# Kernel optimization log

Hardware: AMD Instinct MI355X
Metric: run time of the kernel (lower is better)

Reference implementation:

```python
import jax, jax.numpy as jnp
import numpy as np

BN_EPS = 1e-5


def setup_inputs() -> dict:
    key = jax.random.key(0)
    ks = jax.random.split(key, 3)
    B, S, C, H, W = 4, 8, 64, 96, 96
    P = 6
    DIM = 768
    x = jax.random.normal(ks[0], (B, S, C, H, W), dtype=jnp.float32)
    conv_w = jax.random.normal(ks[1], (C, C, 3, 3), dtype=jnp.float32) * 0.05
    conv_b = jnp.zeros((C,), dtype=jnp.float32)
    bn_gamma = jnp.ones((C,), dtype=jnp.float32)
    bn_beta = jnp.zeros((C,), dtype=jnp.float32)
    bn_mean = jnp.zeros((C,), dtype=jnp.float32)
    bn_var = jnp.ones((C,), dtype=jnp.float32)
    proj_w = jax.random.normal(ks[2], (DIM, P * P * C), dtype=jnp.float32) * 0.02
    proj_b = jnp.zeros((DIM,), dtype=jnp.float32)
    mask = jnp.ones((P, P), dtype=jnp.float32)
    return {"x": x, "conv_w": conv_w, "conv_b": conv_b,
            "bn_gamma": bn_gamma, "bn_beta": bn_beta,
            "bn_mean": bn_mean, "bn_var": bn_var,
            "proj_w": proj_w, "proj_b": proj_b,
            "mask": mask, "patch_size": P}


def reference(x, conv_w, conv_b, bn_gamma, bn_beta, bn_mean, bn_var,
              proj_w, proj_b, mask, patch_size):
    B, S, C, H, W = x.shape
    p = patch_size
    Cout = conv_w.shape[0]
    # Fuse the per-frame loop: run conv over all B*S frames at once.
    xf = x.reshape(B * S, C, H, W)
    y = jax.lax.conv_general_dilated(
        xf, conv_w, window_strides=(1, 1), padding=[(1, 1), (1, 1)],
        dimension_numbers=("NCHW", "OIHW", "NCHW"))
    y = y + conv_b[None, :, None, None]
    # BatchNorm2d (eval-mode running stats); Dropout2d is identity at eval.
    inv = jax.lax.rsqrt(bn_var + BN_EPS)
    y = (y - bn_mean[None, :, None, None]) * (bn_gamma * inv)[None, :, None, None] \
        + bn_beta[None, :, None, None]
    y = jax.nn.gelu(y, approximate=False)  # torch GELU default = exact erf
    y = y.reshape(B, S, Cout, H, W)
    # Patch extraction, row-major over (l_idx, r_idx) exactly as the loop.
    pr = H // p  # patches per row
    patches = y.reshape(B, S, Cout, pr, p, pr, p).transpose(0, 1, 3, 5, 2, 4, 6)
    patches = patches.reshape(B, S, pr * pr, Cout, p, p) * mask  # [B,S,P,C,p,p]
    # Flatten(start_dim=2 on [B,S,C,p,p]) + Linear + GELU, batched over patches.
    flat = patches.reshape(B, S, pr * pr, Cout * p * p)
    tokens = jax.nn.gelu(
        jnp.einsum("bsnf,df->bsnd", flat, proj_w) + proj_b, approximate=False)
    return tokens, patches
```

## Files before the change

kernel.cpp:

```cpp
#include <hip/hip_runtime.h>
#include <hip/hip_bf16.h>
#include <math.h>


typedef unsigned short u16;
typedef __bf16 bf16x8 __attribute__((ext_vector_type(8)));
typedef float f32x4 __attribute__((ext_vector_type(4)));

#define NFRM 32
#define CH 64
#define HW 96
#define HWP 98
#define KP 2304
#define DIMN 768
#define MTOK 8192
#define TOKN (MTOK * DIMN)
#define NPAT (MTOK * KP)
#define XHWC_ELEMS ((size_t)NFRM * HWP * HWP * CH)
#define BP_OFF XHWC_ELEMS
#define PW_OFF (BP_OFF + 36864)

static __device__ __forceinline__ u16 f2b(float f) {
  unsigned u = __builtin_bit_cast(unsigned, f);
  u += 0x7fffu + ((u >> 16) & 1u);
  return (u16)(u >> 16);
}
static __device__ __forceinline__ float gelu_f(float x) {
  return 0.5f * x * (1.0f + erff(x * 0.7071067811865476f));
}

__global__ __launch_bounds__(256) void k_transpose(const float* __restrict__ x,
                                                   u16* __restrict__ xhwc) {
  __shared__ u16 tile[96 * 66];
  const int f = blockIdx.x / 96, h = blockIdx.x % 96;
  const int t = threadIdx.x;
  const float* xp = x + (size_t)f * CH * HW * HW + (size_t)h * HW;
#pragma unroll
  for (int k = 0; k < 6; ++k) {
    int e = (k * 256 + t) * 4;
    int ci = e / 96, w = e % 96;
    float4 v = *(const float4*)(xp + (size_t)ci * (HW * HW) + w);
    tile[(w + 0) * 66 + ci] = f2b(v.x);
    tile[(w + 1) * 66 + ci] = f2b(v.y);
    tile[(w + 2) * 66 + ci] = f2b(v.z);
    tile[(w + 3) * 66 + ci] = f2b(v.w);
  }
  __syncthreads();
  u16* op = xhwc + ((size_t)(f * HWP + h + 1) * HWP + 1) * CH;
#pragma unroll
  for (int k = 0; k < 12; ++k) {
    int e2 = (k * 256 + t) * 2;
    int w = e2 >> 6, ci = e2 & 63;
    *(unsigned*)(op + e2) = *(const unsigned*)(&tile[w * 66 + ci]);
  }
}

__global__ __launch_bounds__(256) void k_bpack(const float* __restrict__ w,
                                               u16* __restrict__ bp) {
  int e = blockIdx.x * 256 + threadIdx.x;
  int co = e / 576, r = e - co * 576, tap = r >> 6, ci = r & 63;
  bp[e] = f2b(w[(co * 64 + ci) * 9 + tap]);
}

__global__ __launch_bounds__(256) void k_pw(const float* __restrict__ pw,
                                            u16* __restrict__ dst) {
  int e = (blockIdx.x * 256 + threadIdx.x) * 4;
  float4 v = *(const float4*)(pw + e);
  ushort4 o;
  o.x = f2b(v.x); o.y = f2b(v.y); o.z = f2b(v.z); o.w = f2b(v.w);
  *(ushort4*)(dst + e) = o;
}

__global__ __launch_bounds__(256) void k_conv(
    const u16* __restrict__ xhwc, const u16* __restrict__ bw,
    const float* __restrict__ cb, const float* __restrict__ gma,
    const float* __restrict__ bta, const float* __restrict__ mu,
    const float* __restrict__ var, const float* __restrict__ msk,
    float* __restrict__ pout) {
  __shared__ u16 As[128 * 72];
  __shared__ u16 Bs[64 * 72];
  const int f = blockIdx.x / 72;
  const int m0 = (blockIdx.x % 72) * 128;
  const int t = threadIdx.x;
  const int wv = t >> 6, l = t & 63, quad = l >> 4, lm = l & 15;

  const int r = t >> 1, c0 = (t & 1) * 32;
  const int mg = m0 + r;
  const int np = mg / 36, ii = mg - np * 36;
  const int hb = (np >> 4) * 6 + ii / 6;
  const int wb = (np & 15) * 6 + (ii % 6);
  const u16* xf = xhwc + (size_t)f * (HWP * HWP * CH);
  const int bco = t >> 2, bc = (t & 3) * 16;

  f32x4 acc[2][4];
#pragma unroll
  for (int s = 0; s < 2; ++s)
#pragma unroll
    for (int u = 0; u < 4; ++u) acc[s][u] = (f32x4){0.f, 0.f, 0.f, 0.f};

  for (int tap = 0; tap < 9; ++tap) {
    const int di = tap / 3, dj = tap - di * 3;
    __syncthreads();
    const u16* src = xf + ((hb + di) * HWP + (wb + dj)) * CH + c0;
    u16* dA = &As[r * 72 + c0];
    *(uint4*)(dA + 0) = *(const uint4*)(src + 0);
    *(uint4*)(dA + 8) = *(const uint4*)(src + 8);
    *(uint4*)(dA + 16) = *(const uint4*)(src + 16);
    *(uint4*)(dA + 24) = *(const uint4*)(src + 24);
    const u16* bsrc = bw + bco * 576 + tap * 64 + bc;
    u16* dB = &Bs[bco * 72 + bc];
    *(uint4*)(dB + 0) = *(const uint4*)(bsrc + 0);
    *(uint4*)(dB + 8) = *(const uint4*)(bsrc + 8);
    __syncthreads();
#pragma unroll
    for (int ks = 0; ks < 2; ++ks) {
      const int ko = ks * 32 + quad * 8;
      bf16x8 a0 = *(const bf16x8*)&As[(wv * 32 + lm) * 72 + ko];
      bf16x8 a1 = *(const bf16x8*)&As[(wv * 32 + 16 + lm) * 72 + ko];
#pragma unroll
      for (int u = 0; u < 4; ++u) {
        bf16x8 b = *(const bf16x8*)&Bs[(u * 16 + lm) * 72 + ko];
        acc[0][u] = __builtin_amdgcn_mfma_f32_16x16x32_bf16(a0, b, acc[0][u], 0, 0, 0);
        acc[1][u] = __builtin_amdgcn_mfma_f32_16x16x32_bf16(a1, b, acc[1][u], 0, 0, 0);
      }
    }
  }
  const int mwb = m0 + wv * 32;
#pragma unroll
  for (int u = 0; u < 4; ++u) {
    const int co = u * 16 + lm;
    const float scv = gma[co] * rsqrtf(var[co] + 1e-5f);
    const float b2v = (cb[co] - mu[co]) * scv + bta[co];
#pragma unroll
    for (int s = 0; s < 2; ++s) {
#pragma unroll
      for (int rg = 0; rg < 4; ++rg) {
        const int ml = mwb + s * 16 + quad * 4 + rg;
        const int n = ml / 36, jj = ml - n * 36;
        float v = acc[s][u][rg] * scv + b2v;
        v = gelu_f(v) * msk[jj];
        pout[((size_t)(f * 256 + n) * 64 + co) * 36 + jj] = v;
      }
    }
  }
}

__global__ __launch_bounds__(256) void k_cvt(const float* __restrict__ pat,
                                             u16* __restrict__ abf) {
  int e = (blockIdx.x * 256 + threadIdx.x) * 4;
  float4 v = *(const float4*)(pat + e);
  ushort4 o;
  o.x = f2b(v.x); o.y = f2b(v.y); o.z = f2b(v.z); o.w = f2b(v.w);
  *(ushort4*)(abf + e) = o;
}

__global__ __launch_bounds__(256) void k_gemm(const u16* __restrict__ A,
                                              const u16* __restrict__ Bt,
                                              const float* __restrict__ pb,
                                              float* __restrict__ out) {
  __shared__ u16 As[128 * 40];
  __shared__ u16 Bs[64 * 40];
  const int bn = blockIdx.x % 12, bm = blockIdx.x / 12;
  const int m0 = bm * 128, n0 = bn * 64;
  const int t = threadIdx.x, wv = t >> 6, l = t & 63, quad = l >> 4, lm = l & 15;
  const int ar = t >> 2, ac = (t & 3) * 8;

  f32x4 acc[2][4];
#pragma unroll
  for (int s = 0; s < 2; ++s)
#pragma unroll
    for (int u = 0; u < 4; ++u) acc[s][u] = (f32x4){0.f, 0.f, 0.f, 0.f};

  for (int k0 = 0; k0 < KP; k0 += 32) {
    __syncthreads();
    *(uint4*)&As[ar * 40 + ac] = *(const uint4*)&A[(size_t)(m0 + ar) * KP + k0 + ac];
    *(uint4*)&As[(ar + 64) * 40 + ac] =
        *(const uint4*)&A[(size_t)(m0 + ar + 64) * KP + k0 + ac];
    *(uint4*)&Bs[ar * 40 + ac] = *(const uint4*)&Bt[(size_t)(n0 + ar) * KP + k0 + ac];
    __syncthreads();
    const int ko = quad * 8;
    bf16x8 a0 = *(const bf16x8*)&As[(wv * 32 + lm) * 40 + ko];
    bf16x8 a1 = *(const bf16x8*)&As[(wv * 32 + 16 + lm) * 40 + ko];
#pragma unroll
    for (int u = 0; u < 4; ++u) {
      bf16x8 b = *(const bf16x8*)&Bs[(u * 16 + lm) * 40 + ko];
      acc[0][u] = __builtin_amdgcn_mfma_f32_16x16x32_bf16(a0, b, acc[0][u], 0, 0, 0);
      acc[1][u] = __builtin_amdgcn_mfma_f32_16x16x32_bf16(a1, b, acc[1][u], 0, 0, 0);
    }
  }
#pragma unroll
  for (int u = 0; u < 4; ++u) {
    const int n = n0 + u * 16 + lm;
    const float bias = pb[n];
#pragma unroll
    for (int s = 0; s < 2; ++s) {
#pragma unroll
      for (int rg = 0; rg < 4; ++rg) {
        const int m = m0 + wv * 32 + s * 16 + quad * 4 + rg;
        out[(size_t)m * DIMN + n] = gelu_f(acc[s][u][rg] + bias);
      }
    }
  }
}

extern "C" void kernel_launch(void* const* d_in, const int* in_sizes, int n_in,
                              void* d_out, int out_size, void* d_ws, size_t ws_size,
                              hipStream_t stream) {
  const float* x = (const float*)d_in[0];
  const float* conv_w = (const float*)d_in[1];
  const float* conv_b = (const float*)d_in[2];
  const float* bn_gamma = (const float*)d_in[3];
  const float* bn_beta = (const float*)d_in[4];
  const float* bn_mean = (const float*)d_in[5];
  const float* bn_var = (const float*)d_in[6];
  const float* proj_w = (const float*)d_in[7];
  const float* proj_b = (const float*)d_in[8];
  const float* mask = (const float*)d_in[9];
  float* out = (float*)d_out;
  float* patches = out + TOKN;
  u16* ws = (u16*)d_ws;
  u16* xhwc = ws;
  u16* bp = ws + BP_OFF;
  u16* pw = ws + PW_OFF;

  hipMemsetAsync(d_ws, 0, XHWC_ELEMS * sizeof(u16), stream);
  k_transpose<<<NFRM * HW, 256, 0, stream>>>(x, xhwc);
  k_bpack<<<144, 256, 0, stream>>>(conv_w, bp);
  k_pw<<<1728, 256, 0, stream>>>(proj_w, pw);
  k_conv<<<NFRM * 72, 256, 0, stream>>>(xhwc, bp, conv_b, bn_gamma, bn_beta,
                                        bn_mean, bn_var, mask, patches);
  k_cvt<<<18432, 256, 0, stream>>>(patches, xhwc);
  k_gemm<<<64 * 12, 256, 0, stream>>>(xhwc, pw, proj_b, out);
}
```

Before: 329.9 us.

## Restructure conv to stage full halo row-band in LDS and use direct global-to-LDS loads

The conv kernel now loads an 8-row by 98-column halo band of the padded NHWC input once into XOR-swizzled LDS using global_load_lds. It then reuses that band across all 9 taps with 512-thread blocks and a larger per-wave tile, so input pixels are no longer re-fetched from global memory for every tap. Conv weights are staged in two tap blocks. The projection GEMM also switches its A/B tile staging to direct global-to-LDS loads with unpadded LDS rows. The larger LDS footprint and register tile may limit occupancy, and the unpadded GEMM tiles may cause LDS bank conflicts.

```diff
diff --git a/kernel.cpp b/kernel.cpp
--- a/kernel.cpp
+++ b/kernel.cpp
@@ -19,6 +19,7 @@
 #define XHWC_ELEMS ((size_t)NFRM * HWP * HWP * CH)
 #define BP_OFF XHWC_ELEMS
 #define PW_OFF (BP_OFF + 36864)
+#define BSTR 328
 
 static __device__ __forceinline__ u16 f2b(float f) {
   unsigned u = __builtin_bit_cast(unsigned, f);
@@ -27,6 +28,12 @@
 }
 static __device__ __forceinline__ float gelu_f(float x) {
   return 0.5f * x * (1.0f + erff(x * 0.7071067811865476f));
+}
+
+typedef __attribute__((address_space(3))) unsigned int lds_uint;
+typedef __attribute__((address_space(1))) const unsigned int g_uint;
+static __device__ __forceinline__ void gload16(const u16* g, u16* s) {
+  __builtin_amdgcn_global_load_lds((g_uint*)g, (lds_uint*)s, 16, 0, 0);
 }
 
 __global__ __launch_bounds__(256) void k_transpose(const float* __restrict__ x,
@@ -71,73 +78,88 @@
   *(ushort4*)(dst + e) = o;
 }
 
-__global__ __launch_bounds__(256) void k_conv(
+template <int T0, int NT>
+static __device__ __forceinline__ void conv_tapblock(
+    const u16* __restrict__ bw, u16* Bs2, const char* asb,
+    f32x4 (&acc)[9][2], const int (&pb)[9],
+    const int t, const int wn, const int lm, const int quad) {
+  for (int e = t; e < 64 * NT * 8; e += 512) {
+    const int co = e / (NT * 8), kk = e - co * (NT * 8);
+    *(uint4*)&Bs2[co * BSTR + kk * 8] = *(const uint4*)&bw[co * 576 + T0 * 64 + kk * 8];
+  }
+  __syncthreads();
+#pragma unroll
+  for (int tp = 0; tp < NT; ++tp) {
+    const int tap = T0 + tp;
+    const int di = tap / 3, dj = tap - (tap / 3) * 3;
+#pragma unroll
+    for (int ks = 0; ks < 2; ++ks) {
+      const int kq = ks * 4 + quad;
+      const bf16x8 b0 = *(const bf16x8*)&Bs2[(wn * 32 + lm) * BSTR + tp * 64 + ks * 32 + quad * 8];
+      const bf16x8 b1 = *(const bf16x8*)&Bs2[(wn * 32 + 16 + lm) * BSTR + tp * 64 + ks * 32 + quad * 8];
+#pragma unroll
+      for (int mf = 0; mf < 9; ++mf) {
+        const int p = pb[mf] + di * 98 + dj;
+        const bf16x8 a = *(const bf16x8*)(asb + p * 128 + ((kq ^ (p & 7)) << 4));
+        acc[mf][0] = __builtin_amdgcn_mfma_f32_16x16x32_bf16(a, b0, acc[mf][0], 0, 0, 0);
+        acc[mf][1] = __builtin_amdgcn_mfma_f32_16x16x32_bf16(a, b1, acc[mf][1], 0, 0, 0);
+      }
+    }
+  }
+}
+
+__global__ __launch_bounds__(512, 2) void k_conv(
     const u16* __restrict__ xhwc, const u16* __restrict__ bw,
     const float* __restrict__ cb, const float* __restrict__ gma,
     const float* __restrict__ bta, const float* __restrict__ mu,
     const float* __restrict__ var, const float* __restrict__ msk,
     float* __restrict__ pout) {
-  __shared__ u16 As[128 * 72];
-  __shared__ u16 Bs[64 * 72];
-  const int f = blockIdx.x / 72;
-  const int m0 = (blockIdx.x % 72) * 128;
+  __shared__ alignas(16) u16 As2[8 * 98 * 64];
+  __shared__ alignas(16) u16 Bs2[64 * BSTR];
+  const int f = blockIdx.x >> 4, pr0 = blockIdx.x & 15;
   const int t = threadIdx.x;
-  const int wv = t >> 6, l = t & 63, quad = l >> 4, lm = l & 15;
-
-  const int r = t >> 1, c0 = (t & 1) * 32;
-  const int mg = m0 + r;
-  const int np = mg / 36, ii = mg - np * 36;
-  const int hb = (np >> 4) * 6 + ii / 6;
-  const int wb = (np & 15) * 6 + (ii % 6);
-  const u16* xf = xhwc + (size_t)f * (HWP * HWP * CH);
-  const int bco = t >> 2, bc = (t & 3) * 16;
-
-  f32x4 acc[2][4];
-#pragma unroll
-  for (int s = 0; s < 2; ++s)
-#pragma unroll
-    for (int u = 0; u < 4; ++u) acc[s][u] = (f32x4){0.f, 0.f, 0.f, 0.f};
-
-  for (int tap = 0; tap < 9; ++tap) {
-    const int di = tap / 3, dj = tap - di * 3;
-    __syncthreads();
-    const u16* src = xf + ((hb + di) * HWP + (wb + dj)) * CH + c0;
-    u16* dA = &As[r * 72 + c0];
-    *(uint4*)(dA + 0) = *(const uint4*)(src + 0);
-    *(uint4*)(dA + 8) = *(const uint4*)(src + 8);
-    *(uint4*)(dA + 16) = *(const uint4*)(src + 16);
-    *(uint4*)(dA + 24) = *(const uint4*)(src + 24);
-    const u16* bsrc = bw + bco * 576 + tap * 64 + bc;
-    u16* dB = &Bs[bco * 72 + bc];
-    *(uint4*)(dB + 0) = *(const uint4*)(bsrc + 0);
-    *(uint4*)(dB + 8) = *(const uint4*)(bsrc + 8);
-    __syncthreads();
-#pragma unroll
-    for (int ks = 0; ks < 2; ++ks) {
-      const int ko = ks * 32 + quad * 8;
-      bf16x8 a0 = *(const bf16x8*)&As[(wv * 32 + lm) * 72 + ko];
-      bf16x8 a1 = *(const bf16x8*)&As[(wv * 32 + 16 + lm) * 72 + ko];
-#pragma unroll
-      for (int u = 0; u < 4; ++u) {
-        bf16x8 b = *(const bf16x8*)&Bs[(u * 16 + lm) * 72 + ko];
-        acc[0][u] = __builtin_amdgcn_mfma_f32_16x16x32_bf16(a0, b, acc[0][u], 0, 0, 0);
-        acc[1][u] = __builtin_amdgcn_mfma_f32_16x16x32_bf16(a1, b, acc[1][u], 0, 0, 0);
-      }
-    }
-  }
-  const int mwb = m0 + wv * 32;
-#pragma unroll
-  for (int u = 0; u < 4; ++u) {
-    const int co = u * 16 + lm;
+  const int wid = t >> 6, l = t & 63, quad = l >> 4, lm = l & 15;
+  const int wm = wid >> 1, wn = wid & 1;
+
+  const u16* sbase = xhwc + ((size_t)f * HWP + pr0 * 6) * (HWP * CH);
+  for (int c = wid; c < 98; c += 8) {
+    const int p = c * 8 + (l >> 3);
+    const int g = (l & 7) ^ (p & 7);
+    gload16(sbase + p * 64 + g * 8, &As2[c * 512]);
+  }
+
+  int pb[9];
+#pragma unroll
+  for (int mf = 0; mf < 9; ++mf) {
+    const int i16 = wm * 9 + mf;
+    pb[mf] = (i16 / 6) * 98 + (i16 % 6) * 16 + lm;
+  }
+  f32x4 acc[9][2];
+#pragma unroll
+  for (int mf = 0; mf < 9; ++mf) {
+    acc[mf][0] = (f32x4){0.f, 0.f, 0.f, 0.f};
+    acc[mf][1] = (f32x4){0.f, 0.f, 0.f, 0.f};
+  }
+  const char* asb = (const char*)As2;
+
+  conv_tapblock<0, 5>(bw, Bs2, asb, acc, pb, t, wn, lm, quad);
+  __syncthreads();
+  conv_tapblock<5, 4>(bw, Bs2, asb, acc, pb, t, wn, lm, quad);
+
+#pragma unroll
+  for (int nf = 0; nf < 2; ++nf) {
+    const int co = wn * 32 + nf * 16 + lm;
     const float scv = gma[co] * rsqrtf(var[co] + 1e-5f);
     const float b2v = (cb[co] - mu[co]) * scv + bta[co];
 #pragma unroll
-    for (int s = 0; s < 2; ++s) {
+    for (int mf = 0; mf < 9; ++mf) {
 #pragma unroll
       for (int rg = 0; rg < 4; ++rg) {
-        const int ml = mwb + s * 16 + quad * 4 + rg;
-        const int n = ml / 36, jj = ml - n * 36;
-        float v = acc[s][u][rg] * scv + b2v;
+        const int ml = wm * 144 + mf * 16 + quad * 4 + rg;
+        const int rr = ml / 96, w = ml - rr * 96;
+        const int n = pr0 * 16 + w / 6;
+        const int jj = rr * 6 + (w - (w / 6) * 6);
+        float v = acc[mf][nf][rg] * scv + b2v;
         v = gelu_f(v) * msk[jj];
         pout[((size_t)(f * 256 + n) * 64 + co) * 36 + jj] = v;
       }
@@ -158,12 +180,19 @@
                                               const u16* __restrict__ Bt,
                                               const float* __restrict__ pb,
                                               float* __restrict__ out) {
-  __shared__ u16 As[128 * 40];
-  __shared__ u16 Bs[64 * 40];
+  __shared__ alignas(16) u16 As[128 * 32];
+  __shared__ alignas(16) u16 Bs[64 * 32];
   const int bn = blockIdx.x % 12, bm = blockIdx.x / 12;
   const int m0 = bm * 128, n0 = bn * 64;
   const int t = threadIdx.x, wv = t >> 6, l = t & 63, quad = l >> 4, lm = l & 15;
-  const int ar = t >> 2, ac = (t & 3) * 8;
+
+  const int crow = l >> 2, cg = (l & 3) * 8;
+  const u16* aS0 = A + (size_t)(m0 + wv * 32 + crow) * KP + cg;
+  const u16* aS1 = A + (size_t)(m0 + wv * 32 + 16 + crow) * KP + cg;
+  const u16* bS = Bt + (size_t)(n0 + wv * 16 + crow) * KP + cg;
+  u16* aD0 = &As[wv * 1024];
+  u16* aD1 = &As[wv * 1024 + 512];
+  u16* bD = &Bs[wv * 512];
 
   f32x4 acc[2][4];
 #pragma unroll
@@ -173,17 +202,16 @@
 
   for (int k0 = 0; k0 < KP; k0 += 32) {
     __syncthreads();
-    *(uint4*)&As[ar * 40 + ac] = *(const uint4*)&A[(size_t)(m0 + ar) * KP + k0 + ac];
-    *(uint4*)&As[(ar + 64) * 40 + ac] =
-        *(const uint4*)&A[(size_t)(m0 + ar + 64) * KP + k0 + ac];
-    *(uint4*)&Bs[ar * 40 + ac] = *(const uint4*)&Bt[(size_t)(n0 + ar) * KP + k0 + ac];
+    gload16(aS0 + k0, aD0);
+    gload16(aS1 + k0, aD1);
+    gload16(bS + k0, bD);
     __syncthreads();
     const int ko = quad * 8;
-    bf16x8 a0 = *(const bf16x8*)&As[(wv * 32 + lm) * 40 + ko];
-    bf16x8 a1 = *(const bf16x8*)&As[(wv * 32 + 16 + lm) * 40 + ko];
+    const bf16x8 a0 = *(const bf16x8*)&As[(wv * 32 + lm) * 32 + ko];
+    const bf16x8 a1 = *(const bf16x8*)&As[(wv * 32 + 16 + lm) * 32 + ko];
 #pragma unroll
     for (int u = 0; u < 4; ++u) {
-      bf16x8 b = *(const bf16x8*)&Bs[(u * 16 + lm) * 40 + ko];
+      const bf16x8 b = *(const bf16x8*)&Bs[(u * 16 + lm) * 32 + ko];
       acc[0][u] = __builtin_amdgcn_mfma_f32_16x16x32_bf16(a0, b, acc[0][u], 0, 0, 0);
       acc[1][u] = __builtin_amdgcn_mfma_f32_16x16x32_bf16(a1, b, acc[1][u], 0, 0, 0);
     }
@@ -227,7 +255,7 @@
   k_transpose<<<NFRM * HW, 256, 0, stream>>>(x, xhwc);
   k_bpack<<<144, 256, 0, stream>>>(conv_w, bp);
   k_pw<<<1728, 256, 0, stream>>>(proj_w, pw);
-  k_conv<<<NFRM * 72, 256, 0, stream>>>(xhwc, bp, conv_b, bn_gamma, bn_beta,
+  k_conv<<<NFRM * 16, 512, 0, stream>>>(xhwc, bp, conv_b, bn_gamma, bn_beta,
                                         bn_mean, bn_var, mask, patches);
   k_cvt<<<18432, 256, 0, stream>>>(patches, xhwc);
   k_gemm<<<64 * 12, 256, 0, stream>>>(xhwc, pw, proj_b, out);
```

Result: slower. 356.6 us (+8.1%).
